# Optimization experiments

Hardware: AMD Instinct MI355X
Metric: run time of the kernel (lower is better)

## Reference

```python
import jax, jax.numpy as jnp
import numpy as np

B, F, HIST, FUT, L = 512, 1024, 20, 30, 3


def setup_inputs() -> dict:
    key = jax.random.key(0)
    k0, k1, k2 = jax.random.split(key, 3)
    # xavier_normal with gain 0.9 for [4F, F] weights: std = gain*sqrt(2/(fan_in+fan_out))
    std = 0.9 * np.sqrt(2.0 / (4 * F + F)).astype(np.float32)
    seq_input = jax.random.normal(k0, (B, F, HIST), jnp.float32)
    Wih = jax.random.normal(k1, (L, 4 * F, F), jnp.float32) * std
    Whh = jax.random.normal(k2, (L, 4 * F, F), jnp.float32) * std
    bih = jnp.zeros((L, 4 * F), jnp.float32)
    bhh = jnp.zeros((L, 4 * F), jnp.float32)
    return {"seq_input": seq_input, "Wih": Wih, "Whh": Whh,
            "bih": bih, "bhh": bhh, "fut_len": FUT}


def _lstm_cell(x, h, c, Wih, Whh, bih, bhh):
    # torch.nn.LSTMCell math, gate order i, f, g, o
    gates = x @ Wih.T + bih + h @ Whh.T + bhh  # [B, 4F]
    i, f, g, o = jnp.split(gates, 4, axis=-1)
    c_new = jax.nn.sigmoid(f) * c + jax.nn.sigmoid(i) * jnp.tanh(g)
    h_new = jax.nn.sigmoid(o) * jnp.tanh(c_new)
    return h_new, c_new


def _stack_step(h, c, x, Wih, Whh, bih, bhh):
    # h, c: [L, B, F]; x: [B, F]. Python loop over L=3 layers only.
    nL = Wih.shape[0]
    hs, cs = [], []
    inp = x
    for l in range(nL):
        h_l, c_l = _lstm_cell(inp, h[l], c[l], Wih[l], Whh[l], bih[l], bhh[l])
        hs.append(h_l)
        cs.append(c_l)
        inp = h_l
    return jnp.stack(hs), jnp.stack(cs)


def reference(seq_input, Wih, Whh, bih, bhh, fut_len):
    b, f, _ = seq_input.shape
    nL = Wih.shape[0]
    h0 = jnp.zeros((nL, b, f), seq_input.dtype)
    c0 = jnp.zeros((nL, b, f), seq_input.dtype)
    xs = jnp.transpose(seq_input, (2, 0, 1))  # [hist_len, B, F]

    def hist_step(carry, x):
        h, c = carry
        h, c = _stack_step(h, c, x, Wih, Whh, bih, bhh)
        return (h, c), None

    (h, c), _ = jax.lax.scan(hist_step, (h0, c0), xs)

    def fut_step(carry, _):
        h, c, x = carry
        h, c = _stack_step(h, c, x, Wih, Whh, bih, bhh)
        y = h[-1]  # recurrent_input = top-layer hidden state
        return (h, c, y), y

    # first decoder input is the top-layer CELL state after history
    _, ys = jax.lax.scan(fut_step, (h, c, c[-1]), None, length=fut_len)
    return jnp.transpose(ys, (1, 2, 0))  # [B, F, fut_len]
```

## Files before the change

kernel.cpp:

```cpp
#include <hip/hip_runtime.h>


#define BDIM 512
#define FDIM 1024
#define HISTLEN 20
#define LAYERS 3
#define NG 4096
#define KD 1024
#define KSTEPS 16

typedef __attribute__((ext_vector_type(8))) short short8;
typedef __attribute__((ext_vector_type(4))) float f32x4;
typedef __attribute__((ext_vector_type(4))) unsigned short u16x4;

__device__ __forceinline__ float sigf(float x) { return 1.f / (1.f + __expf(-x)); }
__device__ __forceinline__ float tanh_fast(float x) {
    float e = __expf(-2.f * fabsf(x));
    float r = (1.f - e) / (1.f + e);
    return copysignf(r, x);
}
__device__ __forceinline__ ushort bfhi(float w) { return (ushort)(__float_as_uint(w) >> 16); }
__device__ __forceinline__ float hif(float w) { return __uint_as_float(__float_as_uint(w) & 0xFFFF0000u); }
__device__ __forceinline__ ushort bflo(float w) { return bfhi(w - hif(w)); }

__device__ __forceinline__ void gl16(const ushort* g, ushort* l) {
    __builtin_amdgcn_global_load_lds(
        (const __attribute__((address_space(1))) unsigned int*)g,
        (__attribute__((address_space(3))) unsigned int*)l, 16, 0, 0);
}

__global__ void prep_w(const float* __restrict__ Wih, const float* __restrict__ Whh,
                       ushort* __restrict__ Whi, ushort* __restrict__ Wlo)
{
    size_t i4 = ((size_t)blockIdx.x * 256 + threadIdx.x) * 4;
    size_t slot = i4 >> 22;
    size_t off  = i4 & 0x3FFFFFu;
    const float* src = ((slot & 1) ? Whh : Wih) + ((slot >> 1) << 22) + off;
    float4 v = *(const float4*)src;
    u16x4 hi, lo;
    #pragma unroll
    for (int e = 0; e < 4; ++e) {
        float w = ((const float*)&v)[e];
        unsigned u = __float_as_uint(w);
        hi[e] = (ushort)(u >> 16);
        float r = w - __uint_as_float(u & 0xFFFF0000u);
        lo[e] = (ushort)(__float_as_uint(r) >> 16);
    }
    *(u16x4*)(Whi + i4) = hi;
    *(u16x4*)(Wlo + i4) = lo;
}

__global__ __launch_bounds__(256, 2) void gemm_split(
    const ushort* __restrict__ A0hi, const ushort* __restrict__ A0lo,
    const ushort* __restrict__ W0hi, const ushort* __restrict__ W0lo,
    const ushort* __restrict__ A1hi, const ushort* __restrict__ A1lo,
    const ushort* __restrict__ W1hi, const ushort* __restrict__ W1lo,
    float* __restrict__ gp)
{
    __shared__ __attribute__((aligned(16))) ushort lds[2][4][4096];

    const int z  = blockIdx.z;
    const int s  = z & 1;
    const int kh = z >> 1;
    const ushort* Ahi = s ? A1hi : A0hi;
    const ushort* Alo = s ? A1lo : A0lo;
    const ushort* Whi = s ? W1hi : W0hi;
    const ushort* Wlo = s ? W1lo : W0lo;
    float* out = gp + (size_t)z * BDIM * NG;

    const int tid = threadIdx.x;
    const int m0 = blockIdx.y * 128;
    const int n0 = blockIdx.x * 128;

    const int srow = tid >> 2;
    const int sc   = tid & 3;
    const int sf   = (srow >> 1) & 3;
    const int scol = (sc ^ sf) << 3;
    const int kbeg = kh * (KD / 2);

    const ushort* pAhi = Ahi + (size_t)(m0 + srow) * KD + kbeg + scol;
    const ushort* pAlo = Alo + (size_t)(m0 + srow) * KD + kbeg + scol;
    const ushort* pWhi = Whi + (size_t)(n0 + srow) * KD + kbeg + scol;
    const ushort* pWlo = Wlo + (size_t)(n0 + srow) * KD + kbeg + scol;
    const int rstep = 64 * KD;

    const int lane = tid & 63;
    const int wid  = tid >> 6;
    const int wm = (wid & 1) * 64;
    const int wn = (wid >> 1) * 64;
    const int frow = lane & 15;
    const int oct  = lane >> 4;

    int a_e[4], w_e[4];
    #pragma unroll
    for (int i = 0; i < 4; ++i) {
        int ra = wm + i * 16 + frow;
        a_e[i] = ra * 32 + (((oct ^ (ra >> 1)) & 3) << 3);
        int rw = wn + i * 16 + frow;
        w_e[i] = rw * 32 + (((oct ^ (rw >> 1)) & 3) << 3);
    }

    f32x4 acc[4][4] = {};

    auto STAGE = [&](ushort* buf, int kk) {
        ushort* d0 = buf + tid * 8;
        gl16(pAhi + kk,         d0);
        gl16(pAlo + kk,         d0 + 4096);
        gl16(pWhi + kk,         d0 + 8192);
        gl16(pWlo + kk,         d0 + 12288);
        ushort* d1 = d0 + 2048;
        gl16(pAhi + rstep + kk, d1);
        gl16(pAlo + rstep + kk, d1 + 4096);
        gl16(pWhi + rstep + kk, d1 + 8192);
        gl16(pWlo + rstep + kk, d1 + 12288);
    };

    auto COMPUTE = [&](const ushort* buf) {
        short8 fah[4], fal[4], fbh[4], fbl[4];
        #pragma unroll
        for (int i = 0; i < 4; ++i) {
            fah[i] = *(const short8*)(buf + a_e[i]);
            fal[i] = *(const short8*)(buf + 4096 + a_e[i]);
            fbh[i] = *(const short8*)(buf + 8192 + w_e[i]);
            fbl[i] = *(const short8*)(buf + 12288 + w_e[i]);
        }
        asm volatile("s_waitcnt lgkmcnt(0)" ::: "memory");
        __builtin_amdgcn_sched_barrier(0);
        __builtin_amdgcn_s_barrier();
        __builtin_amdgcn_sched_barrier(0);
        __builtin_amdgcn_s_setprio(1);
        #pragma unroll
        for (int j = 0; j < 4; ++j) {
            #pragma unroll
            for (int i = 0; i < 4; ++i) {
                acc[i][j] = __builtin_amdgcn_mfma_f32_16x16x32_bf16(fah[i], fbh[j], acc[i][j], 0, 0, 0);
                acc[i][j] = __builtin_amdgcn_mfma_f32_16x16x32_bf16(fal[i], fbh[j], acc[i][j], 0, 0, 0);
                acc[i][j] = __builtin_amdgcn_mfma_f32_16x16x32_bf16(fah[i], fbl[j], acc[i][j], 0, 0, 0);
            }
        }
        __builtin_amdgcn_s_setprio(0);
    };

    STAGE(&lds[0][0][0], 0);
    #pragma unroll 1
    for (int t = 0; t < KSTEPS - 1; ++t) {
        STAGE(&lds[(t + 1) & 1][0][0], (t + 1) * 32);
        asm volatile("s_waitcnt vmcnt(8)" ::: "memory");
        __builtin_amdgcn_sched_barrier(0);
        __builtin_amdgcn_s_barrier();
        __builtin_amdgcn_sched_barrier(0);
        COMPUTE(&lds[t & 1][0][0]);
    }
    asm volatile("s_waitcnt vmcnt(0)" ::: "memory");
    __builtin_amdgcn_s_barrier();
    COMPUTE(&lds[(KSTEPS - 1) & 1][0][0]);

    #pragma unroll
    for (int i = 0; i < 4; ++i) {
        #pragma unroll
        for (int j = 0; j < 4; ++j) {
            int col = n0 + wn + j * 16 + frow;
            #pragma unroll
            for (int r = 0; r < 4; ++r) {
                int row = m0 + wm + i * 16 + oct * 4 + r;
                out[(size_t)row * NG + col] = acc[i][j][r];
            }
        }
    }
}

__global__ void cell_fuse(const float* __restrict__ gp,
                          const float* __restrict__ bi, const float* __restrict__ bh,
                          float* __restrict__ c,
                          ushort* __restrict__ Hhi, ushort* __restrict__ Hlo,
                          float* __restrict__ y, int t, int fut)
{
    const size_t MN = (size_t)BDIM * NG;
    int idx = blockIdx.x * blockDim.x + threadIdx.x;
    int b = idx >> 10, f = idx & 1023;
    const float* g0 = gp + (size_t)b * NG;
    const float* g1 = g0 + MN;
    const float* g2 = g1 + MN;
    const float* g3 = g2 + MN;
    float ig = g0[f] + g1[f] + g2[f] + g3[f] + bi[f] + bh[f];
    float fg = g0[FDIM + f] + g1[FDIM + f] + g2[FDIM + f] + g3[FDIM + f]
             + bi[FDIM + f] + bh[FDIM + f];
    float gg = g0[2 * FDIM + f] + g1[2 * FDIM + f] + g2[2 * FDIM + f] + g3[2 * FDIM + f]
             + bi[2 * FDIM + f] + bh[2 * FDIM + f];
    float og = g0[3 * FDIM + f] + g1[3 * FDIM + f] + g2[3 * FDIM + f] + g3[3 * FDIM + f]
             + bi[3 * FDIM + f] + bh[3 * FDIM + f];
    float cn = sigf(fg) * c[idx] + sigf(ig) * tanh_fast(gg);
    float hn = sigf(og) * tanh_fast(cn);
    c[idx] = cn;
    Hhi[idx] = bfhi(hn);
    Hlo[idx] = bflo(hn);
    if (y) y[(size_t)idx * fut + t] = hn;
}

__global__ void pack_split(const float* __restrict__ seq,
                           ushort* __restrict__ Xhi, ushort* __restrict__ Xlo, int t)
{
    int idx = blockIdx.x * blockDim.x + threadIdx.x;
    float v = seq[(size_t)idx * HISTLEN + t];
    Xhi[idx] = bfhi(v);
    Xlo[idx] = bflo(v);
}

__global__ void split_vec(const float* __restrict__ src,
                          ushort* __restrict__ hi, ushort* __restrict__ lo)
{
    int idx = blockIdx.x * blockDim.x + threadIdx.x;
    float v = src[idx];
    hi[idx] = bfhi(v);
    lo[idx] = bflo(v);
}

extern "C" void kernel_launch(void* const* d_in, const int* in_sizes, int n_in,
                              void* d_out, int out_size, void* d_ws, size_t ws_size,
                              hipStream_t stream)
{
    const float* seq = (const float*)d_in[0];
    const float* Wih = (const float*)d_in[1];
    const float* Whh = (const float*)d_in[2];
    const float* bih = (const float*)d_in[3];
    const float* bhh = (const float*)d_in[4];
    float* out = (float*)d_out;

    const int fut = out_size / (BDIM * FDIM);
    const size_t BF = (size_t)BDIM * FDIM;
    const size_t MN = (size_t)BDIM * NG;
    const size_t Wsl = (size_t)1 << 22;

    float*  c   = (float*)d_ws;
    ushort* Hhi = (ushort*)(c + LAYERS * BF);
    ushort* Hlo = Hhi + LAYERS * BF;
    ushort* Xhi = Hlo + LAYERS * BF;
    ushort* Xlo = Xhi + BF;
    float*  gp  = (float*)(Xlo + BF);
    ushort* Whi = (ushort*)(gp + 4 * MN);
    ushort* Wlo = Whi + 6 * Wsl;

    const size_t need = (size_t)((char*)(Wlo + 6 * Wsl) - (char*)d_ws);
    if (ws_size < need) return;

    hipMemsetAsync(d_ws, 0, LAYERS * BF * 8, stream);
    prep_w<<<24576, 256, 0, stream>>>(Wih, Whh, Whi, Wlo);

    dim3 ggrid(NG / 128, BDIM / 128, 4);
    const int cgrid = (int)(BF / 256);

    for (int t = 0; t < HISTLEN + fut; ++t) {
        const bool dec = (t >= HISTLEN);
        if (!dec) {
            pack_split<<<cgrid, 256, 0, stream>>>(seq, Xhi, Xlo, t);
        } else if (t == HISTLEN) {
            split_vec<<<cgrid, 256, 0, stream>>>(c + 2 * BF, Xhi, Xlo);
        }
        for (int l = 0; l < LAYERS; ++l) {
            const ushort* axh;
            const ushort* axl;
            if (l > 0)        { axh = Hhi + (size_t)(l - 1) * BF; axl = Hlo + (size_t)(l - 1) * BF; }
            else if (!dec || t == HISTLEN) { axh = Xhi; axl = Xlo; }
            else              { axh = Hhi + 2 * BF; axl = Hlo + 2 * BF; }

            gemm_split<<<ggrid, 256, 0, stream>>>(
                axh, axl, Whi + (size_t)(2 * l) * Wsl, Wlo + (size_t)(2 * l) * Wsl,
                Hhi + (size_t)l * BF, Hlo + (size_t)l * BF,
                Whi + (size_t)(2 * l + 1) * Wsl, Wlo + (size_t)(2 * l + 1) * Wsl,
                gp);

            cell_fuse<<<cgrid, 256, 0, stream>>>(
                gp, bih + l * NG, bhh + l * NG,
                c + (size_t)l * BF, Hhi + (size_t)l * BF, Hlo + (size_t)l * BF,
                (dec && l == LAYERS - 1) ? out : nullptr, dec ? t - HISTLEN : 0, fut);
        }
    }
}
```

Before: 5.827 ms.

## Enlarge GEMM tiles to 256x256 with 512 threads and raise split-K to four

The split-bf16 GEMM now uses 256x256 output tiles computed by 8 waves, each wave owning a 128x64 sub-tile. B fragments are loaded per column inside the MFMA loop, and the block barrier moves to the end of each compute step. The K dimension is split four ways per weight matrix, giving eight partial-sum slabs that cell_fuse reduces in a loop. The larger tiles aim to cut global and LDS traffic per FLOP. The cost is twice the partial-sum write and read traffic, higher register pressure with a risk of spills, 128KB of LDS that allows only one block per CU, and a grid of just 256 blocks.

```diff
diff --git a/kernel.cpp b/kernel.cpp
--- a/kernel.cpp
+++ b/kernel.cpp
@@ -7,7 +7,8 @@
 #define LAYERS 3
 #define NG 4096
 #define KD 1024
-#define KSTEPS 16
+#define KSTEPS 8
+#define NZ 8
 
 typedef __attribute__((ext_vector_type(8))) short short8;
 typedef __attribute__((ext_vector_type(4))) float f32x4;
@@ -50,14 +51,14 @@
     *(u16x4*)(Wlo + i4) = lo;
 }
 
-__global__ __launch_bounds__(256, 2) void gemm_split(
+__global__ __launch_bounds__(512, 2) void gemm_split(
     const ushort* __restrict__ A0hi, const ushort* __restrict__ A0lo,
     const ushort* __restrict__ W0hi, const ushort* __restrict__ W0lo,
     const ushort* __restrict__ A1hi, const ushort* __restrict__ A1lo,
     const ushort* __restrict__ W1hi, const ushort* __restrict__ W1lo,
     float* __restrict__ gp)
 {
-    __shared__ __attribute__((aligned(16))) ushort lds[2][4][4096];
+    __shared__ __attribute__((aligned(16))) ushort lds[2][4 * 8192];
 
     const int z  = blockIdx.z;
     const int s  = z & 1;
@@ -69,94 +70,92 @@
     float* out = gp + (size_t)z * BDIM * NG;
 
     const int tid = threadIdx.x;
-    const int m0 = blockIdx.y * 128;
-    const int n0 = blockIdx.x * 128;
+    const int m0 = blockIdx.y * 256;
+    const int n0 = blockIdx.x * 256;
 
     const int srow = tid >> 2;
-    const int sc   = tid & 3;
-    const int sf   = (srow >> 1) & 3;
-    const int scol = (sc ^ sf) << 3;
-    const int kbeg = kh * (KD / 2);
+    const int scol = ((tid & 3) ^ ((srow >> 1) & 3)) << 3;
+    const int kbeg = kh * 256;
 
     const ushort* pAhi = Ahi + (size_t)(m0 + srow) * KD + kbeg + scol;
     const ushort* pAlo = Alo + (size_t)(m0 + srow) * KD + kbeg + scol;
     const ushort* pWhi = Whi + (size_t)(n0 + srow) * KD + kbeg + scol;
     const ushort* pWlo = Wlo + (size_t)(n0 + srow) * KD + kbeg + scol;
-    const int rstep = 64 * KD;
+    const int rstep = 128 * KD;
 
     const int lane = tid & 63;
     const int wid  = tid >> 6;
-    const int wm = (wid & 1) * 64;
-    const int wn = (wid >> 1) * 64;
+    const int wm = (wid >> 2) * 128;
+    const int wn = (wid & 3) * 64;
     const int frow = lane & 15;
     const int oct  = lane >> 4;
 
-    int a_e[4], w_e[4];
-    #pragma unroll
-    for (int i = 0; i < 4; ++i) {
+    int a_e[8], w_e[4];
+    #pragma unroll
+    for (int i = 0; i < 8; ++i) {
         int ra = wm + i * 16 + frow;
         a_e[i] = ra * 32 + (((oct ^ (ra >> 1)) & 3) << 3);
-        int rw = wn + i * 16 + frow;
-        w_e[i] = rw * 32 + (((oct ^ (rw >> 1)) & 3) << 3);
-    }
-
-    f32x4 acc[4][4] = {};
+    }
+    #pragma unroll
+    for (int j = 0; j < 4; ++j) {
+        int rw = wn + j * 16 + frow;
+        w_e[j] = rw * 32 + (((oct ^ (rw >> 1)) & 3) << 3);
+    }
+
+    f32x4 acc[8][4] = {};
 
     auto STAGE = [&](ushort* buf, int kk) {
         ushort* d0 = buf + tid * 8;
         gl16(pAhi + kk,         d0);
-        gl16(pAlo + kk,         d0 + 4096);
-        gl16(pWhi + kk,         d0 + 8192);
-        gl16(pWlo + kk,         d0 + 12288);
-        ushort* d1 = d0 + 2048;
+        gl16(pAlo + kk,         d0 + 8192);
+        gl16(pWhi + kk,         d0 + 16384);
+        gl16(pWlo + kk,         d0 + 24576);
+        ushort* d1 = d0 + 4096;
         gl16(pAhi + rstep + kk, d1);
-        gl16(pAlo + rstep + kk, d1 + 4096);
-        gl16(pWhi + rstep + kk, d1 + 8192);
-        gl16(pWlo + rstep + kk, d1 + 12288);
+        gl16(pAlo + rstep + kk, d1 + 8192);
+        gl16(pWhi + rstep + kk, d1 + 16384);
+        gl16(pWlo + rstep + kk, d1 + 24576);
     };
 
     auto COMPUTE = [&](const ushort* buf) {
-        short8 fah[4], fal[4], fbh[4], fbl[4];
-        #pragma unroll
-        for (int i = 0; i < 4; ++i) {
+        short8 fah[8], fal[8];
+        #pragma unroll
+        for (int i = 0; i < 8; ++i) {
             fah[i] = *(const short8*)(buf + a_e[i]);
-            fal[i] = *(const short8*)(buf + 4096 + a_e[i]);
-            fbh[i] = *(const short8*)(buf + 8192 + w_e[i]);
-            fbl[i] = *(const short8*)(buf + 12288 + w_e[i]);
-        }
-        asm volatile("s_waitcnt lgkmcnt(0)" ::: "memory");
-        __builtin_amdgcn_sched_barrier(0);
+            fal[i] = *(const short8*)(buf + 8192 + a_e[i]);
+        }
+        __builtin_amdgcn_s_setprio(1);
+        #pragma unroll
+        for (int j = 0; j < 4; ++j) {
+            short8 fbh = *(const short8*)(buf + 16384 + w_e[j]);
+            short8 fbl = *(const short8*)(buf + 24576 + w_e[j]);
+            #pragma unroll
+            for (int i = 0; i < 8; ++i) {
+                acc[i][j] = __builtin_amdgcn_mfma_f32_16x16x32_bf16(fah[i], fbh, acc[i][j], 0, 0, 0);
+                acc[i][j] = __builtin_amdgcn_mfma_f32_16x16x32_bf16(fal[i], fbh, acc[i][j], 0, 0, 0);
+                acc[i][j] = __builtin_amdgcn_mfma_f32_16x16x32_bf16(fah[i], fbl, acc[i][j], 0, 0, 0);
+            }
+        }
+        __builtin_amdgcn_s_setprio(0);
         __builtin_amdgcn_s_barrier();
-        __builtin_amdgcn_sched_barrier(0);
-        __builtin_amdgcn_s_setprio(1);
-        #pragma unroll
-        for (int j = 0; j < 4; ++j) {
-            #pragma unroll
-            for (int i = 0; i < 4; ++i) {
-                acc[i][j] = __builtin_amdgcn_mfma_f32_16x16x32_bf16(fah[i], fbh[j], acc[i][j], 0, 0, 0);
-                acc[i][j] = __builtin_amdgcn_mfma_f32_16x16x32_bf16(fal[i], fbh[j], acc[i][j], 0, 0, 0);
-                acc[i][j] = __builtin_amdgcn_mfma_f32_16x16x32_bf16(fah[i], fbl[j], acc[i][j], 0, 0, 0);
-            }
-        }
-        __builtin_amdgcn_s_setprio(0);
     };
 
-    STAGE(&lds[0][0][0], 0);
+    STAGE(&lds[0][0], 0);
     #pragma unroll 1
     for (int t = 0; t < KSTEPS - 1; ++t) {
-        STAGE(&lds[(t + 1) & 1][0][0], (t + 1) * 32);
+        STAGE(&lds[(t + 1) & 1][0], (t + 1) * 32);
         asm volatile("s_waitcnt vmcnt(8)" ::: "memory");
         __builtin_amdgcn_sched_barrier(0);
         __builtin_amdgcn_s_barrier();
         __builtin_amdgcn_sched_barrier(0);
-        COMPUTE(&lds[t & 1][0][0]);
+        COMPUTE(&lds[t & 1][0]);
     }
     asm volatile("s_waitcnt vmcnt(0)" ::: "memory");
     __builtin_amdgcn_s_barrier();
-    COMPUTE(&lds[(KSTEPS - 1) & 1][0][0]);
-
-    #pragma unroll
-    for (int i = 0; i < 4; ++i) {
+    COMPUTE(&lds[(KSTEPS - 1) & 1][0]);
+
+    #pragma unroll
+    for (int i = 0; i < 8; ++i) {
         #pragma unroll
         for (int j = 0; j < 4; ++j) {
             int col = n0 + wn + j * 16 + frow;
@@ -178,19 +177,18 @@
     const size_t MN = (size_t)BDIM * NG;
     int idx = blockIdx.x * blockDim.x + threadIdx.x;
     int b = idx >> 10, f = idx & 1023;
-    const float* g0 = gp + (size_t)b * NG;
-    const float* g1 = g0 + MN;
-    const float* g2 = g1 + MN;
-    const float* g3 = g2 + MN;
-    float ig = g0[f] + g1[f] + g2[f] + g3[f] + bi[f] + bh[f];
-    float fg = g0[FDIM + f] + g1[FDIM + f] + g2[FDIM + f] + g3[FDIM + f]
-             + bi[FDIM + f] + bh[FDIM + f];
-    float gg = g0[2 * FDIM + f] + g1[2 * FDIM + f] + g2[2 * FDIM + f] + g3[2 * FDIM + f]
-             + bi[2 * FDIM + f] + bh[2 * FDIM + f];
-    float og = g0[3 * FDIM + f] + g1[3 * FDIM + f] + g2[3 * FDIM + f] + g3[3 * FDIM + f]
-             + bi[3 * FDIM + f] + bh[3 * FDIM + f];
-    float cn = sigf(fg) * c[idx] + sigf(ig) * tanh_fast(gg);
-    float hn = sigf(og) * tanh_fast(cn);
+    float g4[4];
+    #pragma unroll
+    for (int g = 0; g < 4; ++g) g4[g] = bi[g * FDIM + f] + bh[g * FDIM + f];
+    const float* gz = gp + (size_t)b * NG;
+    #pragma unroll
+    for (int zz = 0; zz < NZ; ++zz) {
+        #pragma unroll
+        for (int g = 0; g < 4; ++g) g4[g] += gz[g * FDIM + f];
+        gz += MN;
+    }
+    float cn = sigf(g4[1]) * c[idx] + sigf(g4[0]) * tanh_fast(g4[2]);
+    float hn = sigf(g4[3]) * tanh_fast(cn);
     c[idx] = cn;
     Hhi[idx] = bfhi(hn);
     Hlo[idx] = bflo(hn);
@@ -237,7 +235,7 @@
     ushort* Xhi = Hlo + LAYERS * BF;
     ushort* Xlo = Xhi + BF;
     float*  gp  = (float*)(Xlo + BF);
-    ushort* Whi = (ushort*)(gp + 4 * MN);
+    ushort* Whi = (ushort*)(gp + NZ * MN);
     ushort* Wlo = Whi + 6 * Wsl;
 
     const size_t need = (size_t)((char*)(Wlo + 6 * Wsl) - (char*)d_ws);
@@ -246,7 +244,7 @@
     hipMemsetAsync(d_ws, 0, LAYERS * BF * 8, stream);
     prep_w<<<24576, 256, 0, stream>>>(Wih, Whh, Whi, Wlo);
 
-    dim3 ggrid(NG / 128, BDIM / 128, 4);
+    dim3 ggrid(NG / 256, BDIM / 256, NZ);
     const int cgrid = (int)(BF / 256);
 
     for (int t = 0; t < HISTLEN + fut; ++t) {
@@ -263,7 +261,7 @@
             else if (!dec || t == HISTLEN) { axh = Xhi; axl = Xlo; }
             else              { axh = Hhi + 2 * BF; axl = Hlo + 2 * BF; }
 
-            gemm_split<<<ggrid, 256, 0, stream>>>(
+            gemm_split<<<ggrid, 512, 0, stream>>>(
                 axh, axl, Whi + (size_t)(2 * l) * Wsl, Wlo + (size_t)(2 * l) * Wsl,
                 Hhi + (size_t)l * BF, Hlo + (size_t)l * BF,
                 Whi + (size_t)(2 * l + 1) * Wsl, Wlo + (size_t)(2 * l + 1) * Wsl,
```

Result: slower. 6.933 ms (+19.0%).
